# Kernel tuning notes

Hardware: AMD Instinct MI355X
Metric: run time of the kernel (lower is better)

Reference implementation:

```python
import jax, jax.numpy as jnp
import numpy as np

SIGMA = 10
POPULATIONS = 2
LR = 0.001


def _normalize(L, prior):
    # clamp then normalize over populations (logsumexp across the population axis)
    O = L.shape[1]
    L = jnp.clip(L, -5.0, 0.0)
    lse = jax.nn.logsumexp(L.reshape(POPULATIONS, -1, O), axis=0)  # (in/P, O)
    L = L - jnp.tile(lse, (POPULATIONS, 1))
    prior = jnp.clip(prior, -5.0, 0.0)
    prior = prior - jax.nn.logsumexp(prior)
    return L, prior


def _forward(x, L, prior):
    B, T, IN = x.shape
    O = L.shape[1]
    L, prior = _normalize(L, prior)  # matches normalize_probs() in __init__

    # membrane potential: OR of spikes over trailing window of SIGMA steps
    xb = x.astype(bool)
    pot = xb
    for s in range(1, SIGMA):  # fixed small loop (sigma=10)
        pot = pot | jnp.pad(xb, ((0, 0), (s, 0), (0, 0)))[:, :T, :]

    tpre0 = jnp.full((B, IN), -T, dtype=jnp.int32)
    tpost0 = jnp.full((B, O), jnp.iinfo(jnp.int32).max, dtype=jnp.int32)
    base_key = jax.random.key(42)

    pot_T = jnp.transpose(pot, (1, 0, 2))  # (T,B,IN)
    x_T = jnp.transpose(xb, (1, 0, 2))

    def step(carry, inp):
        L, prior, tpre, tpost, t = carry
        pot_t, x_t = inp
        potf = pot_t.astype(L.dtype)
        logits = potf @ L + prior  # (B,O), logits <= 0 so exp is safe
        # torch: softmax(exp(logits)).multinomial == categorical with logits=exp(logits)
        key = jax.random.fold_in(base_key, t)
        widx = jax.random.categorical(key, jnp.exp(logits), axis=-1)  # (B,)
        win = jax.nn.one_hot(widx, O, dtype=L.dtype)
        # trace updates happen BEFORE STDP, as in the torch code
        tpre = jnp.where(x_t, 0, tpre - 1)
        tpost = jnp.where(win > 0, 0, tpost - 1)
        ltp = (tpre >= -SIGMA).astype(L.dtype)
        ltd = (tpre < -SIGMA).astype(L.dtype)
        post = (tpost < 0).astype(L.dtype)
        m_ltp = jnp.einsum('bi,bo->io', ltp, win) / B
        m_ltd = jnp.einsum('bi,bo->io', ltd, win) / B
        m_pp = jnp.einsum('bi,bo->io', potf, post) / B
        decay = (t + 1).astype(L.dtype)  # lr_decay_inverse starts at 1
        # dw = (5 e^{-L} - 1) * LTP.mean - LTD.mean - pre_post.mean ; LTD was negated
        dw = (5.0 * jnp.exp(-L) - 1.0) * m_ltp + m_ltd - m_pp
        L2 = L + (LR / decay) * dw
        wm = jnp.mean(win, axis=0)
        db = (-5.0 * prior - 1.0) * wm - (1.0 - wm)
        p2 = prior + (LR / decay) * db
        L2, p2 = _normalize(L2, p2)
        return (L2, p2, tpre, tpost, t + 1), None

    (Lf, pf, _, _, _), _ = jax.lax.scan(
        step, (L, prior, tpre0, tpost0, jnp.int32(0)), (pot_T, x_T))
    return jnp.concatenate([Lf.reshape(-1), pf])


def setup_inputs() -> dict:
    key = jax.random.key(0)
    k1, k2, k3 = jax.random.split(key, 3)
    B, T, IN, O = 256, 200, 1568, 100
    x = jax.random.randint(k1, (B, T, IN), 0, 2, dtype=jnp.int32)
    log_likelihood = jax.random.uniform(k2, (IN, O), dtype=jnp.float32) * -1.0 - 1.0
    log_prior = jax.random.uniform(k3, (O,), dtype=jnp.float32) * -1.0 - 1.0
    return {"x": x, "log_likelihood": log_likelihood, "log_prior": log_prior}


def reference(x, log_likelihood, log_prior):
    return _forward(x, log_likelihood, log_prior)
```

## Files before the change

kernel.cpp:

```cpp
#include <hip/hip_runtime.h>
#include <stdint.h>

#define BB 256
#define TT 200
#define INN 1568
#define OO 100
#define PAIRS 784
#define NHALF 12800

typedef unsigned long long u64;
typedef __attribute__((ext_vector_type(4))) int v4i;

__device__ __forceinline__ void tf_round(uint32_t& x0, uint32_t& x1, int r) {
    x0 += x1;
    x1 = (x1 << r) | (x1 >> (32 - r));
    x1 ^= x0;
}

__device__ __forceinline__ void threefry(uint32_t k0, uint32_t k1,
                                         uint32_t x0, uint32_t x1,
                                         uint32_t& o0, uint32_t& o1) {
    uint32_t k2 = k0 ^ k1 ^ 0x1BD11BDAu;
    x0 += k0; x1 += k1;
    tf_round(x0,x1,13); tf_round(x0,x1,15); tf_round(x0,x1,26); tf_round(x0,x1,6);
    x0 += k1; x1 += k2 + 1u;
    tf_round(x0,x1,17); tf_round(x0,x1,29); tf_round(x0,x1,16); tf_round(x0,x1,24);
    x0 += k2; x1 += k0 + 2u;
    tf_round(x0,x1,13); tf_round(x0,x1,15); tf_round(x0,x1,26); tf_round(x0,x1,6);
    x0 += k0; x1 += k1 + 3u;
    tf_round(x0,x1,17); tf_round(x0,x1,29); tf_round(x0,x1,16); tf_round(x0,x1,24);
    x0 += k1; x1 += k2 + 4u;
    tf_round(x0,x1,13); tf_round(x0,x1,15); tf_round(x0,x1,26); tf_round(x0,x1,6);
    o0 = x0 + k2; o1 = x1 + k0 + 5u;
}

__global__ __launch_bounds__(64) void k_winbit(const int* __restrict__ x,
                                               uint8_t* __restrict__ widx,
                                               u64* __restrict__ bitB) {
    if (blockIdx.x < 800) {
        int idx = blockIdx.x * 64 + threadIdx.x;
        int t = idx >> 8, b = idx & 255;
        uint32_t fk0, fk1;
        threefry(0u, 42u, 0u, (uint32_t)t, fk0, fk1);
        uint32_t bestkey = 0u;
        int bo = 0;
        int nbase = b * OO;
        for (int o = 0; o < OO; ++o) {
            uint32_t n = (uint32_t)(nbase + o);
            uint32_t lo = (n < NHALF) ? n : n - NHALF;
            uint32_t v0, v1;
            threefry(fk0, fk1, lo, lo + NHALF, v0, v1);
            uint32_t bits = (n < NHALF) ? v0 : v1;
            uint32_t key = bits >> 9;
            if (key > bestkey) { bestkey = key; bo = o; }
        }
        widx[idx] = (uint8_t)bo;
    } else {
        int idx = (blockIdx.x - 800) * 64 + threadIdx.x;
        int wb = idx / (TT * 392);
        int r = idx - wb * (TT * 392);
        int t = r / 392;
        int ig = r - t * 392;
        const v4i* xp = (const v4i*)x;
        u64 m0 = 0, m1 = 0, m2 = 0, m3 = 0;
        for (int j = 0; j < 64; ++j) {
            int b = wb * 64 + j;
            v4i v = __builtin_nontemporal_load(&xp[((size_t)b * TT + t) * 392 + ig]);
            u64 bit = 1ull << j;
            if (v.x) m0 |= bit;
            if (v.y) m1 |= bit;
            if (v.z) m2 |= bit;
            if (v.w) m3 |= bit;
        }
        u64* dst = bitB + ((size_t)(t * 4 + wb)) * INN + 4 * ig;
        dst[0] = m0; dst[1] = m1; dst[2] = m2; dst[3] = m3;
    }
}

__global__ __launch_bounds__(256) void k_fwpost(const uint8_t* __restrict__ widx,
                                                u64* __restrict__ winbits,
                                                u64* __restrict__ postbits,
                                                uint32_t* __restrict__ cnt) {
    __shared__ uint32_t wl32[TT * 65];
    __shared__ int fwl[BB];
    int o = blockIdx.x;
    int tid = threadIdx.x;
    const uint32_t* wsrc = (const uint32_t*)widx;
    for (int g = tid; g < TT * 64; g += 256) {
        int t = g >> 6, w = g & 63;
        wl32[t * 65 + w] = wsrc[g];
    }
    __syncthreads();
    if (tid < 64) {
        int f0 = 255, f1 = 255, f2 = 255, f3 = 255;
        for (int t = 0; t < TT; ++t) {
            uint32_t w4 = wl32[t * 65 + tid];
            if (((w4      ) & 255u) == (uint32_t)o && f0 == 255) f0 = t;
            if (((w4 >>  8) & 255u) == (uint32_t)o && f1 == 255) f1 = t;
            if (((w4 >> 16) & 255u) == (uint32_t)o && f2 == 255) f2 = t;
            if (((w4 >> 24) & 255u) == (uint32_t)o && f3 == 255) f3 = t;
        }
        fwl[4 * tid + 0] = f0; fwl[4 * tid + 1] = f1;
        fwl[4 * tid + 2] = f2; fwl[4 * tid + 3] = f3;
    }
    __syncthreads();
    if (tid < TT) {
        int t = tid;
        u64 wbA[4], pbA[4];
        uint32_t c = 0;
        #pragma unroll
        for (int k = 0; k < 4; ++k) {
            u64 wacc = 0, pacc = 0;
            for (int q2 = 0; q2 < 16; ++q2) {
                uint32_t w4 = wl32[t * 65 + k * 16 + q2];
                #pragma unroll
                for (int j = 0; j < 4; ++j) {
                    int bl = q2 * 4 + j;
                    bool win = (((w4 >> (8 * j)) & 255u) == (uint32_t)o);
                    c += win ? 1u : 0u;
                    bool post = (fwl[k * 64 + q2 * 4 + j] < t) && !win;
                    u64 bit = 1ull << bl;
                    if (win)  wacc |= bit;
                    if (post) pacc |= bit;
                }
            }
            wbA[k] = wacc; pbA[k] = pacc;
        }
        size_t base = (size_t)(t * OO + o) * 4;
        #pragma unroll
        for (int k = 0; k < 4; ++k) {
            winbits[base + k] = wbA[k];
            postbits[base + k] = pbA[k];
        }
        cnt[t * OO + o] = c;
    }
}

#define PBLK 16
#define OBLK 20
#define FTHR 320
#define ROWSTRIDE (4 * INN)

__global__ __launch_bounds__(FTHR) void k_fused(
        const float* __restrict__ L0,
        const float* __restrict__ p0arr,
        const u64* __restrict__ bitB,
        const u64* __restrict__ winbits,
        const u64* __restrict__ postbits,
        const uint32_t* __restrict__ cnt,
        float* __restrict__ outL,
        float* __restrict__ outp) {
    if (blockIdx.x == 49) {
        if (blockIdx.y != 0) return;
        int l = threadIdx.x;
        if (l >= 64) return;
        bool has2 = (l + 64) < OO;
        float pa = p0arr[l];
        float pb = has2 ? p0arr[l + 64] : -1e30f;
        auto normalize = [&]() {
            pa = fminf(fmaxf(pa, -5.0f), 0.0f);
            if (has2) pb = fminf(fmaxf(pb, -5.0f), 0.0f);
            float mx = has2 ? fmaxf(pa, pb) : pa;
            #pragma unroll
            for (int s = 32; s > 0; s >>= 1) mx = fmaxf(mx, __shfl_xor(mx, s, 64));
            float sm = expf(pa - mx) + (has2 ? expf(pb - mx) : 0.0f);
            #pragma unroll
            for (int s = 32; s > 0; s >>= 1) sm += __shfl_xor(sm, s, 64);
            float lse = logf(sm) + mx;
            pa -= lse;
            if (has2) pb -= lse;
        };
        normalize();
        for (int t = 0; t < TT; ++t) {
            float eta = 0.001f / (float)(t + 1);
            float wma = (float)cnt[t * OO + l] * (1.0f / 256.0f);
            pa += eta * ((-5.0f * pa - 1.0f) * wma - (1.0f - wma));
            if (has2) {
                float wmb = (float)cnt[t * OO + l + 64] * (1.0f / 256.0f);
                pb += eta * ((-5.0f * pb - 1.0f) * wmb - (1.0f - wmb));
            }
            normalize();
        }
        outp[l] = pa;
        if (has2) outp[l + 64] = pb;
        return;
    }

    __shared__ u64 potL[2][PBLK * 10];
    __shared__ u64 ltpL[2][PBLK * 10];
    __shared__ u64 winL[2][OBLK * 4];
    __shared__ u64 postL[2][OBLK * 4];
    __shared__ float cntL[2][OBLK];

    int tid = threadIdx.x;
    int p0 = blockIdx.x * PBLK;
    int o0 = blockIdx.y * OBLK;
    int pl = tid & 15;
    int ol = tid >> 4;
    int o  = o0 + ol;
    int i0 = p0 + pl;
    int i1 = i0 + PAIRS;

    const u64* colbase = bitB + (size_t)(ol & 3) * INN
                       + ((ol < 8) ? (size_t)(p0 + pl + (ol >> 2) * PAIRS) : 0);
    int s  = tid - 128;
    int ols = s >> 3, js = s & 7;

    if (tid < 128) {
        u64 acc = 0, r0 = 0;
        #pragma unroll
        for (int ii = 0; ii < 11; ++ii) {
            int tt = ii - 10; tt = (tt < 0) ? 0 : tt;
            u64 v = colbase[(size_t)tt * ROWSTRIDE];
            if (ii == 0) r0 = v; else acc |= v;
        }
        potL[0][pl * 10 + ol] = acc;
        ltpL[0][pl * 10 + ol] = acc | r0;
    } else if (tid < 288) {
        size_t base = (size_t)(o0 + ols) * 4;
        if (js < 4) winL[0][ols * 4 + js] = winbits[base + js];
        else        postL[0][ols * 4 + js - 4] = postbits[base + js - 4];
    } else if (tid < 308) {
        cntL[0][tid - 288] = (float)cnt[o0 + (tid - 288)];
    }

    float a  = L0[(size_t)i0 * OO + o];
    float b2 = L0[(size_t)i1 * OO + o];
    a  = fminf(fmaxf(a,  -5.0f), 0.0f);
    b2 = fminf(fmaxf(b2, -5.0f), 0.0f);
    {
        float m = fmaxf(a, b2), mn = fminf(a, b2);
        float lse = __logf(1.0f + __expf(mn - m)) + m;
        a -= lse; b2 -= lse;
    }
    __syncthreads();

    for (int t = 0; t < TT; ++t) {
        int cur = t & 1, nxt = cur ^ 1;
        bool pre = (t + 1 < TT);
        u64 wv[11];
        u64 stg = 0; float cstg = 0.0f;
        if (pre) {
            if (tid < 128) {
                int tb = t + 1 - 10;
                #pragma unroll
                for (int ii = 0; ii < 11; ++ii) {
                    int tt = tb + ii; tt = (tt < 0) ? 0 : tt;
                    wv[ii] = colbase[(size_t)tt * ROWSTRIDE];
                }
            } else if (tid < 288) {
                size_t base = (size_t)((t + 1) * OO + o0 + ols) * 4;
                stg = (js < 4) ? winbits[base + js] : postbits[base + js - 4];
            } else if (tid < 308) {
                cstg = (float)cnt[(t + 1) * OO + o0 + (tid - 288)];
            }
        }
        u64 W0 = winL[cur][ol * 4 + 0], W1 = winL[cur][ol * 4 + 1];
        u64 W2 = winL[cur][ol * 4 + 2], W3 = winL[cur][ol * 4 + 3];
        u64 S0 = postL[cur][ol * 4 + 0], S1 = postL[cur][ol * 4 + 1];
        u64 S2 = postL[cur][ol * 4 + 2], S3 = postL[cur][ol * 4 + 3];
        const u64* Pp = &potL[cur][pl * 10];
        const u64* Lp = &ltpL[cur][pl * 10];
        uint32_t lt0 = __popcll(Lp[0] & W0) + __popcll(Lp[1] & W1)
                     + __popcll(Lp[2] & W2) + __popcll(Lp[3] & W3);
        uint32_t lt1 = __popcll(Lp[4] & W0) + __popcll(Lp[5] & W1)
                     + __popcll(Lp[6] & W2) + __popcll(Lp[7] & W3);
        uint32_t pp0 = __popcll(Pp[0] & S0) + __popcll(Pp[1] & S1)
                     + __popcll(Pp[2] & S2) + __popcll(Pp[3] & S3);
        uint32_t pp1 = __popcll(Pp[4] & S0) + __popcll(Pp[5] & S1)
                     + __popcll(Pp[6] & S2) + __popcll(Pp[7] & S3);
        float cwin = cntL[cur][ol];
        float lt0f = (float)lt0, lt1f = (float)lt1;
        float pp0f = (float)pp0, pp1f = (float)pp1;
        float eta = 0.001f / (float)(t + 1);
        float dw0 = (5.0f * __expf(-a)  - 1.0f) * (lt0f * (1.0f/256.0f))
                  + (cwin - lt0f - pp0f) * (1.0f/256.0f);
        float dw1 = (5.0f * __expf(-b2) - 1.0f) * (lt1f * (1.0f/256.0f))
                  + (cwin - lt1f - pp1f) * (1.0f/256.0f);
        a  += eta * dw0;
        b2 += eta * dw1;
        a  = fminf(fmaxf(a,  -5.0f), 0.0f);
        b2 = fminf(fmaxf(b2, -5.0f), 0.0f);
        float m = fmaxf(a, b2), mn = fminf(a, b2);
        float lse = __logf(1.0f + __expf(mn - m)) + m;
        a -= lse; b2 -= lse;
        if (pre) {
            if (tid < 128) {
                u64 acc = wv[1] | wv[2] | wv[3] | wv[4] | wv[5]
                        | wv[6] | wv[7] | wv[8] | wv[9] | wv[10];
                potL[nxt][pl * 10 + ol] = acc;
                ltpL[nxt][pl * 10 + ol] = acc | wv[0];
            } else if (tid < 288) {
                if (js < 4) winL[nxt][ols * 4 + js] = stg;
                else        postL[nxt][ols * 4 + js - 4] = stg;
            } else if (tid < 308) {
                cntL[nxt][tid - 288] = cstg;
            }
        }
        __syncthreads();
    }
    outL[(size_t)i0 * OO + o] = a;
    outL[(size_t)i1 * OO + o] = b2;
}

extern "C" void kernel_launch(void* const* d_in, const int* in_sizes, int n_in,
                              void* d_out, int out_size, void* d_ws, size_t ws_size,
                              hipStream_t stream) {
    const int*   x  = (const int*)d_in[0];
    const float* L0 = (const float*)d_in[1];
    const float* p0 = (const float*)d_in[2];
    float* out = (float*)d_out;

    char* ws = (char*)d_ws;
    size_t off = 0;
    auto alloc = [&](size_t bytes) -> void* {
        off = (off + 255) & ~(size_t)255;
        void* p = ws + off;
        off += bytes;
        return p;
    };
    uint8_t*  widx     = (uint8_t*) alloc((size_t)TT * BB);
    uint32_t* cnt      = (uint32_t*)alloc((size_t)TT * OO * 4);
    u64*      winbits  = (u64*)     alloc((size_t)TT * OO * 4 * 8);
    u64*      postbits = (u64*)     alloc((size_t)TT * OO * 4 * 8);
    u64*      bitB     = (u64*)     alloc((size_t)TT * 4 * INN * 8);
    (void)ws_size;

    hipLaunchKernelGGL(k_winbit, dim3(800 + 4900), dim3(64), 0, stream, x, widx, bitB);
    hipLaunchKernelGGL(k_fwpost, dim3(OO), dim3(256), 0, stream,
                       widx, winbits, postbits, cnt);
    hipLaunchKernelGGL(k_fused, dim3(50, 5), dim3(FTHR), 0, stream,
                       L0, p0, bitB, winbits, postbits, cnt,
                       out, out + (size_t)INN * OO);
}
```

Baseline: 617.4 us.

## Prefetch per-step bit rows into LDS ring via async global-to-LDS loads

The fused STDP kernel now uses global_load_lds to stream each timestep's bit row, win/post masks and counts into a 16-slot LDS ring, six steps ahead. The sliding-window OR is built from the ring instead of reloading 11 rows from global memory every step. Explicit vmcnt/lgkmcnt waits and a raw s_barrier replace __syncthreads. The bit-packing kernel is also reorganised into 256-thread blocks that each cover two timesteps with contiguous loads. This targets global load latency inside the serial 200-step loop. The manual waitcnt handling is delicate and could break correctness or ordering.

```diff
diff --git a/kernel.cpp b/kernel.cpp
--- a/kernel.cpp
+++ b/kernel.cpp
@@ -10,6 +10,10 @@
 
 typedef unsigned long long u64;
 typedef __attribute__((ext_vector_type(4))) int v4i;
+
+typedef const __attribute__((address_space(1))) uint32_t* gas_p;
+typedef __attribute__((address_space(3))) uint32_t* las_p;
+#define GLD16(g, l) __builtin_amdgcn_global_load_lds((gas_p)(g), (las_p)(l), 16, 0, 0)
 
 __device__ __forceinline__ void tf_round(uint32_t& x0, uint32_t& x1, int r) {
     x0 += x1;
@@ -34,11 +38,12 @@
     o0 = x0 + k2; o1 = x1 + k0 + 5u;
 }
 
-__global__ __launch_bounds__(64) void k_winbit(const int* __restrict__ x,
-                                               uint8_t* __restrict__ widx,
-                                               u64* __restrict__ bitB) {
-    if (blockIdx.x < 800) {
-        int idx = blockIdx.x * 64 + threadIdx.x;
+__global__ __launch_bounds__(256) void k_winbit(const int* __restrict__ x,
+                                                uint8_t* __restrict__ widx,
+                                                u64* __restrict__ bitB) {
+    int tid = threadIdx.x;
+    if (blockIdx.x < 200) {
+        int idx = blockIdx.x * 256 + tid;
         int t = idx >> 8, b = idx & 255;
         uint32_t fk0, fk1;
         threefry(0u, 42u, 0u, (uint32_t)t, fk0, fk1);
@@ -55,25 +60,46 @@
             if (key > bestkey) { bestkey = key; bo = o; }
         }
         widx[idx] = (uint8_t)bo;
-    } else {
-        int idx = (blockIdx.x - 800) * 64 + threadIdx.x;
-        int wb = idx / (TT * 392);
-        int r = idx - wb * (TT * 392);
-        int t = r / 392;
-        int ig = r - t * 392;
-        const v4i* xp = (const v4i*)x;
-        u64 m0 = 0, m1 = 0, m2 = 0, m3 = 0;
-        for (int j = 0; j < 64; ++j) {
-            int b = wb * 64 + j;
-            v4i v = __builtin_nontemporal_load(&xp[((size_t)b * TT + t) * 392 + ig]);
-            u64 bit = 1ull << j;
-            if (v.x) m0 |= bit;
-            if (v.y) m1 |= bit;
-            if (v.z) m2 |= bit;
-            if (v.w) m3 |= bit;
-        }
-        u64* dst = bitB + ((size_t)(t * 4 + wb)) * INN + 4 * ig;
-        dst[0] = m0; dst[1] = m1; dst[2] = m2; dst[3] = m3;
+        return;
+    }
+    int pb = blockIdx.x - 200;
+    int wb = pb / 100;
+    int t0 = (pb - wb * 100) * 2;
+    const v4i* xp = (const v4i*)x;
+    u64 acc[4][4];
+    #pragma unroll
+    for (int q = 0; q < 4; ++q)
+        #pragma unroll
+        for (int c = 0; c < 4; ++c) acc[q][c] = 0;
+    bool x4 = (tid < 16);
+    for (int bl = 0; bl < 64; ++bl) {
+        size_t base = ((size_t)((wb * 64 + bl) * TT + t0)) * 392;
+        u64 bit = 1ull << bl;
+        #pragma unroll
+        for (int q = 0; q < 3; ++q) {
+            v4i v = __builtin_nontemporal_load(&xp[base + tid + q * 256]);
+            if (v.x) acc[q][0] |= bit;
+            if (v.y) acc[q][1] |= bit;
+            if (v.z) acc[q][2] |= bit;
+            if (v.w) acc[q][3] |= bit;
+        }
+        if (x4) {
+            v4i v = __builtin_nontemporal_load(&xp[base + tid + 768]);
+            if (v.x) acc[3][0] |= bit;
+            if (v.y) acc[3][1] |= bit;
+            if (v.z) acc[3][2] |= bit;
+            if (v.w) acc[3][3] |= bit;
+        }
+    }
+    #pragma unroll
+    for (int q = 0; q < 4; ++q) {
+        if (q == 3 && !x4) continue;
+        int p = tid + q * 256;
+        int tp = (p >= 392) ? 1 : 0;
+        int iq = p - tp * 392;
+        u64* dst = bitB + ((size_t)((t0 + tp) * 4 + wb)) * INN + iq * 4;
+        dst[0] = acc[q][0]; dst[1] = acc[q][1];
+        dst[2] = acc[q][2]; dst[3] = acc[q][3];
     }
 }
 
@@ -140,6 +166,8 @@
 #define OBLK 20
 #define FTHR 320
 #define ROWSTRIDE (4 * INN)
+#define PFD 6
+#define RS 16
 
 __global__ __launch_bounds__(FTHR) void k_fused(
         const float* __restrict__ L0,
@@ -186,44 +214,61 @@
         return;
     }
 
-    __shared__ u64 potL[2][PBLK * 10];
-    __shared__ u64 ltpL[2][PBLK * 10];
-    __shared__ u64 winL[2][OBLK * 4];
-    __shared__ u64 postL[2][OBLK * 4];
-    __shared__ float cntL[2][OBLK];
+    __shared__ __align__(16) u64 rowRing[RS][128];
+    __shared__ __align__(16) u64 winRing[RS][80];
+    __shared__ __align__(16) u64 postRing[RS][80];
+    __shared__ __align__(16) uint32_t cntRing[RS][20];
+    __shared__ __align__(16) u64 potL[2][16][10];
+    __shared__ __align__(16) u64 ltpL[2][16][10];
 
     int tid = threadIdx.x;
+    int wave = tid >> 6;
+    int lane = tid & 63;
     int p0 = blockIdx.x * PBLK;
     int o0 = blockIdx.y * OBLK;
+
     int pl = tid & 15;
     int ol = tid >> 4;
     int o  = o0 + ol;
     int i0 = p0 + pl;
     int i1 = i0 + PAIRS;
 
-    const u64* colbase = bitB + (size_t)(ol & 3) * INN
-                       + ((ol < 8) ? (size_t)(p0 + pl + (ol >> 2) * PAIRS) : 0);
-    int s  = tid - 128;
-    int ols = s >> 3, js = s & 7;
-
+    int lk  = lane >> 3;
+    int lpq = (lane & 7) * 2;
+    const u64* rowsrc = bitB + (size_t)((lk & 3) * INN + (lk >> 2) * PAIRS + p0 + lpq);
+
+    int wpl = tid & 15;
+    int wk  = tid >> 4;
+    int eidx = wk * 16 + wpl;
+
+    auto issue = [&](int s) {
+        int rr = (s < TT) ? s : (TT - 1);
+        int slot = s & (RS - 1);
+        if (wave == 0) {
+            GLD16(rowsrc + (size_t)rr * ROWSTRIDE, &rowRing[slot][2 * lane]);
+        } else if (wave == 1) {
+            if (lane < 40)
+                GLD16(winbits + ((size_t)rr * OO + o0) * 4 + 2 * lane,
+                      &winRing[slot][2 * lane]);
+        } else if (wave == 2) {
+            if (lane < 40)
+                GLD16(postbits + ((size_t)rr * OO + o0) * 4 + 2 * lane,
+                      &postRing[slot][2 * lane]);
+        } else if (wave == 3) {
+            if (lane < 5)
+                GLD16(cnt + ((size_t)rr * OO + o0) + 4 * lane,
+                      &cntRing[slot][4 * lane]);
+        }
+    };
+
+    for (int s = 0; s < PFD; ++s) issue(s);
+    if (wave < 4) asm volatile("s_waitcnt vmcnt(0)" ::: "memory");
+    __builtin_amdgcn_s_barrier();
     if (tid < 128) {
-        u64 acc = 0, r0 = 0;
-        #pragma unroll
-        for (int ii = 0; ii < 11; ++ii) {
-            int tt = ii - 10; tt = (tt < 0) ? 0 : tt;
-            u64 v = colbase[(size_t)tt * ROWSTRIDE];
-            if (ii == 0) r0 = v; else acc |= v;
-        }
-        potL[0][pl * 10 + ol] = acc;
-        ltpL[0][pl * 10 + ol] = acc | r0;
-    } else if (tid < 288) {
-        size_t base = (size_t)(o0 + ols) * 4;
-        if (js < 4) winL[0][ols * 4 + js] = winbits[base + js];
-        else        postL[0][ols * 4 + js - 4] = postbits[base + js - 4];
-    } else if (tid < 308) {
-        cntL[0][tid - 288] = (float)cnt[o0 + (tid - 288)];
-    }
-
+        u64 r0 = rowRing[0][eidx];
+        potL[0][wpl][wk] = r0;
+        ltpL[0][wpl][wk] = r0;
+    }
     float a  = L0[(size_t)i0 * OO + o];
     float b2 = L0[(size_t)i1 * OO + o];
     a  = fminf(fmaxf(a,  -5.0f), 0.0f);
@@ -233,34 +278,19 @@
         float lse = __logf(1.0f + __expf(mn - m)) + m;
         a -= lse; b2 -= lse;
     }
-    __syncthreads();
+    asm volatile("s_waitcnt lgkmcnt(0)" ::: "memory");
+    __builtin_amdgcn_s_barrier();
 
     for (int t = 0; t < TT; ++t) {
         int cur = t & 1, nxt = cur ^ 1;
-        bool pre = (t + 1 < TT);
-        u64 wv[11];
-        u64 stg = 0; float cstg = 0.0f;
-        if (pre) {
-            if (tid < 128) {
-                int tb = t + 1 - 10;
-                #pragma unroll
-                for (int ii = 0; ii < 11; ++ii) {
-                    int tt = tb + ii; tt = (tt < 0) ? 0 : tt;
-                    wv[ii] = colbase[(size_t)tt * ROWSTRIDE];
-                }
-            } else if (tid < 288) {
-                size_t base = (size_t)((t + 1) * OO + o0 + ols) * 4;
-                stg = (js < 4) ? winbits[base + js] : postbits[base + js - 4];
-            } else if (tid < 308) {
-                cstg = (float)cnt[(t + 1) * OO + o0 + (tid - 288)];
-            }
-        }
-        u64 W0 = winL[cur][ol * 4 + 0], W1 = winL[cur][ol * 4 + 1];
-        u64 W2 = winL[cur][ol * 4 + 2], W3 = winL[cur][ol * 4 + 3];
-        u64 S0 = postL[cur][ol * 4 + 0], S1 = postL[cur][ol * 4 + 1];
-        u64 S2 = postL[cur][ol * 4 + 2], S3 = postL[cur][ol * 4 + 3];
-        const u64* Pp = &potL[cur][pl * 10];
-        const u64* Lp = &ltpL[cur][pl * 10];
+        issue(t + PFD);
+        int st = t & (RS - 1);
+        u64 W0 = winRing[st][ol * 4 + 0], W1 = winRing[st][ol * 4 + 1];
+        u64 W2 = winRing[st][ol * 4 + 2], W3 = winRing[st][ol * 4 + 3];
+        u64 S0 = postRing[st][ol * 4 + 0], S1 = postRing[st][ol * 4 + 1];
+        u64 S2 = postRing[st][ol * 4 + 2], S3 = postRing[st][ol * 4 + 3];
+        const u64* Pp = potL[cur][pl];
+        const u64* Lp = ltpL[cur][pl];
         uint32_t lt0 = __popcll(Lp[0] & W0) + __popcll(Lp[1] & W1)
                      + __popcll(Lp[2] & W2) + __popcll(Lp[3] & W3);
         uint32_t lt1 = __popcll(Lp[4] & W0) + __popcll(Lp[5] & W1)
@@ -269,7 +299,7 @@
                      + __popcll(Pp[2] & S2) + __popcll(Pp[3] & S3);
         uint32_t pp1 = __popcll(Pp[4] & S0) + __popcll(Pp[5] & S1)
                      + __popcll(Pp[6] & S2) + __popcll(Pp[7] & S3);
-        float cwin = cntL[cur][ol];
+        float cwin = (float)cntRing[st][ol];
         float lt0f = (float)lt0, lt1f = (float)lt1;
         float pp0f = (float)pp0, pp1f = (float)pp1;
         float eta = 0.001f / (float)(t + 1);
@@ -284,20 +314,25 @@
         float m = fmaxf(a, b2), mn = fminf(a, b2);
         float lse = __logf(1.0f + __expf(mn - m)) + m;
         a -= lse; b2 -= lse;
-        if (pre) {
-            if (tid < 128) {
-                u64 acc = wv[1] | wv[2] | wv[3] | wv[4] | wv[5]
-                        | wv[6] | wv[7] | wv[8] | wv[9] | wv[10];
-                potL[nxt][pl * 10 + ol] = acc;
-                ltpL[nxt][pl * 10 + ol] = acc | wv[0];
-            } else if (tid < 288) {
-                if (js < 4) winL[nxt][ols * 4 + js] = stg;
-                else        postL[nxt][ols * 4 + js - 4] = stg;
-            } else if (tid < 308) {
-                cntL[nxt][tid - 288] = cstg;
+        if (tid < 128) {
+            int rbase = t + 1 - 10;
+            u64 acc = 0;
+            #pragma unroll
+            for (int j = 1; j <= 10; ++j) {
+                int rr = rbase + j; if (rr < 0) rr = 0;
+                acc |= rowRing[rr & (RS - 1)][eidx];
             }
-        }
-        __syncthreads();
+            int rz = (rbase < 0) ? 0 : rbase;
+            u64 lt = acc | rowRing[rz & (RS - 1)][eidx];
+            potL[nxt][wpl][wk] = acc;
+            ltpL[nxt][wpl][wk] = lt;
+        }
+        if (wave < 4) {
+            asm volatile("s_waitcnt vmcnt(4) lgkmcnt(0)" ::: "memory");
+        } else {
+            asm volatile("s_waitcnt lgkmcnt(0)" ::: "memory");
+        }
+        __builtin_amdgcn_s_barrier();
     }
     outL[(size_t)i0 * OO + o] = a;
     outL[(size_t)i1 * OO + o] = b2;
@@ -326,7 +361,7 @@
     u64*      bitB     = (u64*)     alloc((size_t)TT * 4 * INN * 8);
     (void)ws_size;
 
-    hipLaunchKernelGGL(k_winbit, dim3(800 + 4900), dim3(64), 0, stream, x, widx, bitB);
+    hipLaunchKernelGGL(k_winbit, dim3(600), dim3(256), 0, stream, x, widx, bitB);
     hipLaunchKernelGGL(k_fwpost, dim3(OO), dim3(256), 0, stream,
                        widx, winbits, postbits, cnt);
     hipLaunchKernelGGL(k_fused, dim3(50, 5), dim3(FTHR), 0, stream,
```

After: 611.6 us. Within noise of the previous version (-0.9%).
